# Kernel tuning notes

Hardware: AMD Instinct MI355X
Metric: run time of the kernel (lower is better)

Reference implementation:

```python
import jax, jax.numpy as jnp
import numpy as np


def setup_inputs() -> dict:
    key = jax.random.key(0)
    k1, k2, k3, k4 = jax.random.split(key, 4)
    N, C, H, W = 4, 256, 64, 64
    Co, kh, kw, dg = 256, 3, 3, 1
    x = jax.random.normal(k1, (N, C, H, W), dtype=jnp.float32)
    offset = jax.random.normal(k2, (N, 2 * dg * kh * kw, H, W), dtype=jnp.float32)
    mask = jax.random.uniform(k3, (N, dg * kh * kw, H, W), dtype=jnp.float32)
    weight = jax.random.normal(k4, (Co, C, kh, kw), dtype=jnp.float32) * 0.02
    bias = jnp.zeros((Co,), dtype=jnp.float32)
    return {"x": x, "offset": offset, "mask": mask, "weight": weight, "bias": bias,
            "stride": 1, "padding": 1, "dilation": 1, "deformable_groups": 1}


def _dcn_v2(x, offset, mask, weight, bias, stride, padding, dilation, dg):
    N, C, H, W = x.shape
    Co, Ci, kh, kw = weight.shape
    K = kh * kw
    Ho, Wo = offset.shape[2], offset.shape[3]
    Cg = C // dg

    off = offset.reshape(N, dg, K, 2, Ho, Wo)
    dy, dx = off[:, :, :, 0], off[:, :, :, 1]          # [N,dg,K,Ho,Wo]
    m = mask.reshape(N, dg, K, Ho, Wo)

    ki = (jnp.arange(K) // kw).astype(jnp.float32)      # kernel row index
    kj = (jnp.arange(K) % kw).astype(jnp.float32)       # kernel col index
    base_y = (jnp.arange(Ho, dtype=jnp.float32) * stride - padding)
    base_x = (jnp.arange(Wo, dtype=jnp.float32) * stride - padding)
    # sampling coordinates [N,dg,K,Ho,Wo]
    py = dy + base_y[None, None, None, :, None] + (ki * dilation)[None, None, :, None, None]
    px = dx + base_x[None, None, None, None, :] + (kj * dilation)[None, None, :, None, None]

    y0 = jnp.floor(py)
    x0 = jnp.floor(px)
    wy1 = py - y0
    wx1 = px - x0
    wy0 = 1.0 - wy1
    wx0 = 1.0 - wx1
    y0i = y0.astype(jnp.int32)
    x0i = x0.astype(jnp.int32)

    xr = x.reshape(N, dg, Cg, H * W)

    def gather(yi, xi):
        valid = ((yi >= 0) & (yi < H) & (xi >= 0) & (xi < W)).astype(x.dtype)
        idx = jnp.clip(yi, 0, H - 1) * W + jnp.clip(xi, 0, W - 1)   # [N,dg,K,Ho,Wo]
        flat = idx.reshape(N, dg, 1, K * Ho * Wo)
        g = jnp.take_along_axis(xr, flat, axis=-1).reshape(N, dg, Cg, K, Ho, Wo)
        return g * valid[:, :, None]

    sampled = (gather(y0i, x0i) * (wy0 * wx0)[:, :, None]
               + gather(y0i, x0i + 1) * (wy0 * wx1)[:, :, None]
               + gather(y0i + 1, x0i) * (wy1 * wx0)[:, :, None]
               + gather(y0i + 1, x0i + 1) * (wy1 * wx1)[:, :, None])
    sampled = sampled * m[:, :, None]                     # modulation
    sampled = sampled.reshape(N, C, K, Ho, Wo)

    out = jnp.einsum('nckhw,ock->nohw', sampled, weight.reshape(Co, C, K))
    return out + bias[None, :, None, None]


def reference(x, offset, mask, weight, bias, stride, padding, dilation, deformable_groups):
    return _dcn_v2(x, offset, mask, weight, bias, stride, padding, dilation, deformable_groups)
```

## Files before the change

kernel.cpp:

```cpp
#include <hip/hip_runtime.h>


typedef _Float16 f16x8 __attribute__((ext_vector_type(8)));
typedef _Float16 f16x4 __attribute__((ext_vector_type(4)));
typedef float f32x4 __attribute__((ext_vector_type(4)));

#define C_IN 256
#define CO   256
#define KK   9
#define HWSZ 4096
#define LDB  72
#define BUFB (64 * LDB)

struct __align__(16) SP2 { uint4 off; f16x4 w; };

static __device__ __forceinline__ f16x8 splat8(_Float16 v) {
    f16x8 r = {v, v, v, v, v, v, v, v};
    return r;
}

__global__ void transpose_x_kernel(const float* __restrict__ x,
                                   _Float16* __restrict__ xt) {
    __shared__ float tile[64][65];
    const int n  = blockIdx.z;
    const int p0 = blockIdx.x * 64;
    const int c0 = blockIdx.y * 64;
    const int tx = threadIdx.x & 63;
    const int ty = threadIdx.x >> 6;
    for (int i = 0; i < 16; ++i) {
        int c = ty * 16 + i;
        tile[c][tx] = x[((size_t)(n * C_IN + c0 + c) << 12) + p0 + tx];
    }
    __syncthreads();
    for (int i = 0; i < 16; ++i) {
        int p = ty * 16 + i;
        xt[((size_t)((n << 12) + p0 + p) << 8) + c0 + tx] = (_Float16)tile[tx][p];
    }
}

__global__ void transpose_w_kernel(const float* __restrict__ w,
                                   _Float16* __restrict__ wt2) {
    const int o = blockIdx.x;
    const int c = threadIdx.x;
    const int f = o >> 4, r = o & 15, cc = c >> 5, kq = c & 31;
    for (int kk = 0; kk < KK; ++kk) {
        int q = cc * 9 + kk;
        wt2[((f * 72 + q) * 16 + r) * 32 + kq] =
            (_Float16)w[(o * C_IN + c) * KK + kk];
    }
}

template <int NHALF>
__launch_bounds__(256, 2)
__global__ void dcn_main_kernel(const float* __restrict__ offset,
                                const float* __restrict__ mask,
                                const float* __restrict__ bias,
                                const _Float16* __restrict__ xt,
                                const _Float16* __restrict__ wt2,
                                float* __restrict__ out0,
                                float* __restrict__ out1) {
    constexpr int NS = 36 / NHALF;
    __shared__ SP2 sP[576];
    __shared__ _Float16 sB[2][BUFB];

    const int tid = threadIdx.x;
    const int cpx = (256 * NHALF) >> 3;
    const int lin = blockIdx.x;
    const int id  = (lin & 7) * cpx + (lin >> 3);
    const int half = (NHALF == 2) ? (id >> 8) : 0;
    const int pt   = id & 255;
    const int p0   = pt * 64;
    const int n    = p0 >> 12;
    const int phw0 = p0 & 4095;
    const int cc0  = half * 4;

    for (int t = tid; t < 576; t += 256) {
        int pl = t / 9;
        int k  = t - pl * 9;
        int phw = phw0 + pl;
        int h = phw >> 6, w = phw & 63;
        float dy = offset[(size_t)(n * 18 + 2 * k)     * HWSZ + phw];
        float dx = offset[(size_t)(n * 18 + 2 * k + 1) * HWSZ + phw];
        float mv = mask  [(size_t)(n * 9 + k)          * HWSZ + phw];
        float py = dy + (float)(h - 1 + k / 3);
        float px = dx + (float)(w - 1 + k % 3);
        float y0f = floorf(py), x0f = floorf(px);
        int y0 = (int)y0f, x0 = (int)x0f;
        float wy1 = py - y0f, wx1 = px - x0f;
        float wy0 = 1.f - wy1, wx0 = 1.f - wx1;
        int y1 = y0 + 1, x1 = x0 + 1;
        float vy0 = (y0 >= 0 && y0 < 64) ? 1.f : 0.f;
        float vy1 = (y1 >= 0 && y1 < 64) ? 1.f : 0.f;
        float vx0 = (x0 >= 0 && x0 < 64) ? 1.f : 0.f;
        float vx1 = (x1 >= 0 && x1 < 64) ? 1.f : 0.f;
        int cy0 = min(max(y0, 0), 63), cy1 = min(max(y1, 0), 63);
        int cx0 = min(max(x0, 0), 63), cx1 = min(max(x1, 0), 63);
        SP2 e;
        e.off = make_uint4((unsigned)(cy0 * 64 + cx0) << 9,
                           (unsigned)(cy0 * 64 + cx1) << 9,
                           (unsigned)(cy1 * 64 + cx0) << 9,
                           (unsigned)(cy1 * 64 + cx1) << 9);
        f16x4 wv;
        wv.x = (_Float16)(wy0 * wx0 * mv * vy0 * vx0);
        wv.y = (_Float16)(wy0 * wx1 * mv * vy0 * vx1);
        wv.z = (_Float16)(wy1 * wx0 * mv * vy1 * vx0);
        wv.w = (_Float16)(wy1 * wx1 * mv * vy1 * vx1);
        e.w = wv;
        sP[t] = e;
    }
    __syncthreads();

    const int lane = tid & 63;
    const int wid  = tid >> 6;
    const int l15  = lane & 15;
    const int lhi  = lane >> 4;

    const int pixl  = tid >> 2;
    const int oct   = tid & 3;
    const int pixl9 = pixl * 9;

    const char* xb  = (const char*)(xt + ((size_t)n << 12) * C_IN);
    const char* wtb = (const char*)wt2;

    const int vBe = l15 * LDB + lhi * 8;
    const int vWe = pixl * LDB + oct * 8;
    const unsigned chBase = (unsigned)(cc0 * 64 + oct * 16);

    unsigned voffA[4];
    for (int fm = 0; fm < 4; ++fm) {
        int fglob = wid * 4 + fm;
        voffA[fm] = (unsigned)((fglob * 72 + cc0 * 9) * 1024 + l15 * 64 + lhi * 16);
    }

    f16x8 ga[2][8];
    f16x8 aa[2][8];
    f16x4 gw[2][2];
    f32x4 acc[4][4];
    for (int i = 0; i < 4; ++i)
        for (int j = 0; j < 4; ++j)
            acc[i][j] = (f32x4){0.f, 0.f, 0.f, 0.f};

#define ISSUE_GA(T, SLOT)                                                     \
    {                                                                         \
        const SP2 e0 = sP[pixl9 + (2 * (T)) % 9];                             \
        const SP2 e1 = sP[pixl9 + (2 * (T) + 1) % 9];                         \
        gw[SLOT][0] = e0.w;                                                   \
        gw[SLOT][1] = e1.w;                                                   \
        const unsigned cE = chBase + (unsigned)(((2 * (T)) / 9) * 64);        \
        const unsigned cO = chBase + (unsigned)(((2 * (T) + 1) / 9) * 64);    \
        ga[SLOT][0] = *(const f16x8*)(xb + (e0.off.x + cE));                  \
        ga[SLOT][1] = *(const f16x8*)(xb + (e0.off.y + cE));                  \
        ga[SLOT][2] = *(const f16x8*)(xb + (e0.off.z + cE));                  \
        ga[SLOT][3] = *(const f16x8*)(xb + (e0.off.w + cE));                  \
        ga[SLOT][4] = *(const f16x8*)(xb + (e1.off.x + cO));                  \
        ga[SLOT][5] = *(const f16x8*)(xb + (e1.off.y + cO));                  \
        ga[SLOT][6] = *(const f16x8*)(xb + (e1.off.z + cO));                  \
        ga[SLOT][7] = *(const f16x8*)(xb + (e1.off.w + cO));                  \
    }

#define ISSUE_A(T, SLOT)                                                      \
    {                                                                         \
        for (int fm_ = 0; fm_ < 4; ++fm_) {                                   \
            unsigned vo_ = voffA[fm_] + (unsigned)((T) * 2048);               \
            aa[SLOT][fm_ * 2 + 0] = *(const f16x8*)(wtb + vo_);               \
            aa[SLOT][fm_ * 2 + 1] = *(const f16x8*)(wtb + vo_ + 1024);        \
        }                                                                     \
    }

#define COMBINE(SLOT, BUF)                                                    \
    {                                                                         \
        _Float16* bw_ = &sB[0][0] + (BUF) * BUFB + vWe;                       \
        f16x8 r0_ = ga[SLOT][0] * splat8(gw[SLOT][0].x)                       \
                  + ga[SLOT][1] * splat8(gw[SLOT][0].y)                       \
                  + ga[SLOT][2] * splat8(gw[SLOT][0].z)                       \
                  + ga[SLOT][3] * splat8(gw[SLOT][0].w);                      \
        f16x8 r1_ = ga[SLOT][4] * splat8(gw[SLOT][1].x)                       \
                  + ga[SLOT][5] * splat8(gw[SLOT][1].y)                       \
                  + ga[SLOT][6] * splat8(gw[SLOT][1].z)                       \
                  + ga[SLOT][7] * splat8(gw[SLOT][1].w);                      \
        *(f16x8*)(bw_)      = r0_;                                            \
        *(f16x8*)(bw_ + 32) = r1_;                                            \
    }

#define MFMA_STEP(SLOT, BUF)                                                  \
    {                                                                         \
        const _Float16* br_ = &sB[0][0] + (BUF) * BUFB + vBe;                 \
        for (int fn_ = 0; fn_ < 4; ++fn_) {                                   \
            f16x8 bE_ = *(const f16x8*)(br_ + fn_ * 16 * LDB);                \
            f16x8 bO_ = *(const f16x8*)(br_ + fn_ * 16 * LDB + 32);           \
            for (int fm_ = 0; fm_ < 4; ++fm_) {                               \
                acc[fm_][fn_] = __builtin_amdgcn_mfma_f32_16x16x32_f16(       \
                    aa[SLOT][fm_ * 2 + 0], bE_, acc[fm_][fn_], 0, 0, 0);      \
                acc[fm_][fn_] = __builtin_amdgcn_mfma_f32_16x16x32_f16(       \
                    aa[SLOT][fm_ * 2 + 1], bO_, acc[fm_][fn_], 0, 0, 0);      \
            }                                                                 \
        }                                                                     \
    }

#define BAR()                                                                 \
    {                                                                         \
        asm volatile("s_waitcnt lgkmcnt(0)" ::: "memory");                    \
        __builtin_amdgcn_s_barrier();                                         \
        asm volatile("" ::: "memory");                                        \
    }

    ISSUE_GA(0, 0)
    ISSUE_GA(1, 1)
    ISSUE_A(0, 0)
    COMBINE(0, 0)
    BAR()

#pragma unroll
    for (int s = 0; s < NS; ++s) {
        if (s + 1 < NS) ISSUE_A(s + 1, (s + 1) & 1)
        if (s + 2 < NS) ISSUE_GA(s + 2, s & 1)
        __builtin_amdgcn_sched_barrier(0);
        MFMA_STEP(s & 1, s & 1)
        if (s + 1 < NS) {
            COMBINE((s + 1) & 1, (s + 1) & 1)
            BAR()
        }
    }

    float* po = (NHALF == 2 && half == 1) ? out1 : out0;
    for (int fm = 0; fm < 4; ++fm) {
        for (int fn = 0; fn < 4; ++fn) {
            int pix = phw0 + fn * 16 + l15;
            for (int r = 0; r < 4; ++r) {
                int o = wid * 64 + fm * 16 + lhi * 4 + r;
                float v = acc[fm][fn][r];
                if constexpr (NHALF == 1) v += bias[o];
                po[((size_t)(n * CO + o) << 12) + pix] = v;
            }
        }
    }
#undef ISSUE_GA
#undef ISSUE_A
#undef COMBINE
#undef MFMA_STEP
#undef BAR
}

__global__ void reduce_kernel(float* __restrict__ out,
                              const float* __restrict__ part,
                              const float* __restrict__ bias, int n4) {
    int i = blockIdx.x * blockDim.x + threadIdx.x;
    const int stride = gridDim.x * blockDim.x;
    for (; i < n4; i += stride) {
        f32x4 a = ((const f32x4*)out)[i];
        f32x4 b = ((const f32x4*)part)[i];
        float bv = bias[(i >> 10) & 255];
        a.x += b.x + bv; a.y += b.y + bv; a.z += b.z + bv; a.w += b.w + bv;
        ((f32x4*)out)[i] = a;
    }
}

extern "C" void kernel_launch(void* const* d_in, const int* in_sizes, int n_in,
                              void* d_out, int out_size, void* d_ws, size_t ws_size,
                              hipStream_t stream) {
    const float* x      = (const float*)d_in[0];
    const float* offset = (const float*)d_in[1];
    const float* mask   = (const float*)d_in[2];
    const float* weight = (const float*)d_in[3];
    const float* bias   = (const float*)d_in[4];
    float* out = (float*)d_out;

    _Float16* xt  = (_Float16*)d_ws;
    _Float16* wt2 = (_Float16*)((char*)d_ws + 8388608);
    float*  part1 = (float*)((char*)d_ws + 9568256);
    const bool split = ws_size >= (size_t)9568256 + (size_t)4 * CO * HWSZ * 4;

    transpose_x_kernel<<<dim3(64, 4, 4), 256, 0, stream>>>(x, xt);
    transpose_w_kernel<<<CO, C_IN, 0, stream>>>(weight, wt2);
    if (split) {
        dcn_main_kernel<2><<<dim3(512), 256, 0, stream>>>(offset, mask, bias,
                                                          xt, wt2, out, part1);
        reduce_kernel<<<dim3(2048), 256, 0, stream>>>(out, part1, bias,
                                                      (4 * CO * HWSZ) / 4);
    } else {
        dcn_main_kernel<1><<<dim3(256), 256, 0, stream>>>(offset, mask, bias,
                                                          xt, wt2, out, out);
    }
}
```

Before: 55.34 us.

## Split channel reduction four ways with fp16 partials and higher occupancy

Raises the split-K factor of the deformable conv GEMM from two to four, launching 1024 blocks so more CUs are busy, and raises launch bounds to target four blocks per SM. All four quarters write fp16 partial sums to workspace, and a one-pass reduce kernel sums them with the bias in fp32. Weight fragments are no longer double-buffered in registers, and MFMA sections get raised wave priority. Storing partials in fp16 adds rounding error and extra reduce traffic, and the lower register budget may cause spills or stalls on the weight loads.

```diff
diff --git a/kernel.cpp b/kernel.cpp
--- a/kernel.cpp
+++ b/kernel.cpp
@@ -11,6 +11,7 @@
 #define HWSZ 4096
 #define LDB  72
 #define BUFB (64 * LDB)
+#define PSTR (4 * CO * HWSZ)
 
 struct __align__(16) SP2 { uint4 off; f16x4 w; };
 
@@ -50,29 +51,29 @@
     }
 }
 
-template <int NHALF>
-__launch_bounds__(256, 2)
+template <int NQ>
+__launch_bounds__(256, 4)
 __global__ void dcn_main_kernel(const float* __restrict__ offset,
                                 const float* __restrict__ mask,
                                 const float* __restrict__ bias,
                                 const _Float16* __restrict__ xt,
                                 const _Float16* __restrict__ wt2,
-                                float* __restrict__ out0,
-                                float* __restrict__ out1) {
-    constexpr int NS = 36 / NHALF;
+                                float* __restrict__ out,
+                                _Float16* __restrict__ parts) {
+    constexpr int NS = 36 / NQ;
     __shared__ SP2 sP[576];
     __shared__ _Float16 sB[2][BUFB];
 
     const int tid = threadIdx.x;
-    const int cpx = (256 * NHALF) >> 3;
+    const int cpx = (256 * NQ) >> 3;
     const int lin = blockIdx.x;
     const int id  = (lin & 7) * cpx + (lin >> 3);
-    const int half = (NHALF == 2) ? (id >> 8) : 0;
+    const int quarter = (NQ > 1) ? (id >> 8) : 0;
     const int pt   = id & 255;
     const int p0   = pt * 64;
     const int n    = p0 >> 12;
     const int phw0 = p0 & 4095;
-    const int cc0  = half * 4;
+    const int cc0  = quarter * (8 / NQ);
 
     for (int t = tid; t < 576; t += 256) {
         int pl = t / 9;
@@ -133,7 +134,7 @@
     }
 
     f16x8 ga[2][8];
-    f16x8 aa[2][8];
+    f16x8 aa[8];
     f16x4 gw[2][2];
     f32x4 acc[4][4];
     for (int i = 0; i < 4; ++i)
@@ -158,12 +159,12 @@
         ga[SLOT][7] = *(const f16x8*)(xb + (e1.off.w + cO));                  \
     }
 
-#define ISSUE_A(T, SLOT)                                                      \
+#define ISSUE_A(T)                                                            \
     {                                                                         \
         for (int fm_ = 0; fm_ < 4; ++fm_) {                                   \
             unsigned vo_ = voffA[fm_] + (unsigned)((T) * 2048);               \
-            aa[SLOT][fm_ * 2 + 0] = *(const f16x8*)(wtb + vo_);               \
-            aa[SLOT][fm_ * 2 + 1] = *(const f16x8*)(wtb + vo_ + 1024);        \
+            aa[fm_ * 2 + 0] = *(const f16x8*)(wtb + vo_);                     \
+            aa[fm_ * 2 + 1] = *(const f16x8*)(wtb + vo_ + 1024);              \
         }                                                                     \
     }
 
@@ -182,19 +183,21 @@
         *(f16x8*)(bw_ + 32) = r1_;                                            \
     }
 
-#define MFMA_STEP(SLOT, BUF)                                                  \
+#define MFMA_STEP(BUF)                                                        \
     {                                                                         \
         const _Float16* br_ = &sB[0][0] + (BUF) * BUFB + vBe;                 \
+        __builtin_amdgcn_s_setprio(1);                                        \
         for (int fn_ = 0; fn_ < 4; ++fn_) {                                   \
             f16x8 bE_ = *(const f16x8*)(br_ + fn_ * 16 * LDB);                \
             f16x8 bO_ = *(const f16x8*)(br_ + fn_ * 16 * LDB + 32);           \
             for (int fm_ = 0; fm_ < 4; ++fm_) {                               \
                 acc[fm_][fn_] = __builtin_amdgcn_mfma_f32_16x16x32_f16(       \
-                    aa[SLOT][fm_ * 2 + 0], bE_, acc[fm_][fn_], 0, 0, 0);      \
+                    aa[fm_ * 2 + 0], bE_, acc[fm_][fn_], 0, 0, 0);            \
                 acc[fm_][fn_] = __builtin_amdgcn_mfma_f32_16x16x32_f16(       \
-                    aa[SLOT][fm_ * 2 + 1], bO_, acc[fm_][fn_], 0, 0, 0);      \
+                    aa[fm_ * 2 + 1], bO_, acc[fm_][fn_], 0, 0, 0);            \
             }                                                                 \
         }                                                                     \
+        __builtin_amdgcn_s_setprio(0);                                        \
     }
 
 #define BAR()                                                                 \
@@ -206,31 +209,42 @@
 
     ISSUE_GA(0, 0)
     ISSUE_GA(1, 1)
-    ISSUE_A(0, 0)
     COMBINE(0, 0)
     BAR()
 
 #pragma unroll
     for (int s = 0; s < NS; ++s) {
-        if (s + 1 < NS) ISSUE_A(s + 1, (s + 1) & 1)
+        ISSUE_A(s)
         if (s + 2 < NS) ISSUE_GA(s + 2, s & 1)
         __builtin_amdgcn_sched_barrier(0);
-        MFMA_STEP(s & 1, s & 1)
+        MFMA_STEP(s & 1)
         if (s + 1 < NS) {
             COMBINE((s + 1) & 1, (s + 1) & 1)
             BAR()
         }
     }
 
-    float* po = (NHALF == 2 && half == 1) ? out1 : out0;
-    for (int fm = 0; fm < 4; ++fm) {
-        for (int fn = 0; fn < 4; ++fn) {
-            int pix = phw0 + fn * 16 + l15;
-            for (int r = 0; r < 4; ++r) {
-                int o = wid * 64 + fm * 16 + lhi * 4 + r;
-                float v = acc[fm][fn][r];
-                if constexpr (NHALF == 1) v += bias[o];
-                po[((size_t)(n * CO + o) << 12) + pix] = v;
+    if constexpr (NQ > 1) {
+        _Float16* pp = parts + (size_t)quarter * PSTR;
+        for (int fm = 0; fm < 4; ++fm) {
+            for (int fn = 0; fn < 4; ++fn) {
+                int pix = phw0 + fn * 16 + l15;
+                for (int r = 0; r < 4; ++r) {
+                    int o = wid * 64 + fm * 16 + lhi * 4 + r;
+                    pp[((size_t)(n * CO + o) << 12) + pix] =
+                        (_Float16)acc[fm][fn][r];
+                }
+            }
+        }
+    } else {
+        for (int fm = 0; fm < 4; ++fm) {
+            for (int fn = 0; fn < 4; ++fn) {
+                int pix = phw0 + fn * 16 + l15;
+                for (int r = 0; r < 4; ++r) {
+                    int o = wid * 64 + fm * 16 + lhi * 4 + r;
+                    out[((size_t)(n * CO + o) << 12) + pix] =
+                        acc[fm][fn][r] + bias[o];
+                }
             }
         }
     }
@@ -242,17 +256,22 @@
 }
 
 __global__ void reduce_kernel(float* __restrict__ out,
-                              const float* __restrict__ part,
-                              const float* __restrict__ bias, int n4) {
+                              const _Float16* __restrict__ parts,
+                              const float* __restrict__ bias, int n8) {
     int i = blockIdx.x * blockDim.x + threadIdx.x;
-    const int stride = gridDim.x * blockDim.x;
-    for (; i < n4; i += stride) {
-        f32x4 a = ((const f32x4*)out)[i];
-        f32x4 b = ((const f32x4*)part)[i];
-        float bv = bias[(i >> 10) & 255];
-        a.x += b.x + bv; a.y += b.y + bv; a.z += b.z + bv; a.w += b.w + bv;
-        ((f32x4*)out)[i] = a;
-    }
+    if (i >= n8) return;
+    f16x8 a = ((const f16x8*)parts)[i];
+    f16x8 b = ((const f16x8*)(parts + PSTR))[i];
+    f16x8 c = ((const f16x8*)(parts + 2 * (size_t)PSTR))[i];
+    f16x8 d = ((const f16x8*)(parts + 3 * (size_t)PSTR))[i];
+    float bv = bias[((i * 8) >> 12) & 255];
+    f32x4 r0, r1;
+    for (int e = 0; e < 4; ++e)
+        r0[e] = (float)a[e] + (float)b[e] + (float)c[e] + (float)d[e] + bv;
+    for (int e = 0; e < 4; ++e)
+        r1[e] = (float)a[e+4] + (float)b[e+4] + (float)c[e+4] + (float)d[e+4] + bv;
+    ((f32x4*)out)[2 * i]     = r0;
+    ((f32x4*)out)[2 * i + 1] = r1;
 }
 
 extern "C" void kernel_launch(void* const* d_in, const int* in_sizes, int n_in,
@@ -267,18 +286,18 @@
 
     _Float16* xt  = (_Float16*)d_ws;
     _Float16* wt2 = (_Float16*)((char*)d_ws + 8388608);
-    float*  part1 = (float*)((char*)d_ws + 9568256);
-    const bool split = ws_size >= (size_t)9568256 + (size_t)4 * CO * HWSZ * 4;
+    _Float16* parts = (_Float16*)((char*)d_ws + 9568256);
+    const bool split = ws_size >= (size_t)9568256 + (size_t)4 * PSTR * 2;
 
     transpose_x_kernel<<<dim3(64, 4, 4), 256, 0, stream>>>(x, xt);
     transpose_w_kernel<<<CO, C_IN, 0, stream>>>(weight, wt2);
     if (split) {
-        dcn_main_kernel<2><<<dim3(512), 256, 0, stream>>>(offset, mask, bias,
-                                                          xt, wt2, out, part1);
-        reduce_kernel<<<dim3(2048), 256, 0, stream>>>(out, part1, bias,
-                                                      (4 * CO * HWSZ) / 4);
+        dcn_main_kernel<4><<<dim3(1024), 256, 0, stream>>>(offset, mask, bias,
+                                                           xt, wt2, out, parts);
+        reduce_kernel<<<dim3(PSTR / 8 / 256), 256, 0, stream>>>(out, parts, bias,
+                                                                PSTR / 8);
     } else {
         dcn_main_kernel<1><<<dim3(256), 256, 0, stream>>>(offset, mask, bias,
-                                                          xt, wt2, out, out);
-    }
-}
+                                                          xt, wt2, out, parts);
+    }
+}
```

Measured after the change: 185.9 us. 236% more time.

## Fuse prep kernels with bias init and replace split-K reduce with atomics

Applied to the files above, without the earlier changes.

Merges the x transpose, weight transpose and a new bias-initialisation of the output into one prep kernel launch. The main kernel always splits the channel reduction into two halves and accumulates directly into the output with float atomicAdd. This drops the partial-sum workspace and the separate reduce kernel. The cost is atomic traffic on every output element plus a full output write during prep, and the summation order becomes nondeterministic.

```diff
diff --git a/kernel.cpp b/kernel.cpp
--- a/kernel.cpp
+++ b/kernel.cpp
@@ -19,55 +19,60 @@
     return r;
 }
 
-__global__ void transpose_x_kernel(const float* __restrict__ x,
-                                   _Float16* __restrict__ xt) {
+__global__ void prep_kernel(const float* __restrict__ x,
+                            const float* __restrict__ w,
+                            const float* __restrict__ bias,
+                            _Float16* __restrict__ xt,
+                            _Float16* __restrict__ wt2,
+                            float* __restrict__ out) {
     __shared__ float tile[64][65];
-    const int n  = blockIdx.z;
-    const int p0 = blockIdx.x * 64;
-    const int c0 = blockIdx.y * 64;
-    const int tx = threadIdx.x & 63;
-    const int ty = threadIdx.x >> 6;
-    for (int i = 0; i < 16; ++i) {
-        int c = ty * 16 + i;
-        tile[c][tx] = x[((size_t)(n * C_IN + c0 + c) << 12) + p0 + tx];
-    }
-    __syncthreads();
-    for (int i = 0; i < 16; ++i) {
-        int p = ty * 16 + i;
-        xt[((size_t)((n << 12) + p0 + p) << 8) + c0 + tx] = (_Float16)tile[tx][p];
-    }
-}
-
-__global__ void transpose_w_kernel(const float* __restrict__ w,
-                                   _Float16* __restrict__ wt2) {
-    const int o = blockIdx.x;
-    const int c = threadIdx.x;
-    const int f = o >> 4, r = o & 15, cc = c >> 5, kq = c & 31;
-    for (int kk = 0; kk < KK; ++kk) {
-        int q = cc * 9 + kk;
-        wt2[((f * 72 + q) * 16 + r) * 32 + kq] =
-            (_Float16)w[(o * C_IN + c) * KK + kk];
-    }
-}
-
-template <int NHALF>
+    const int b = blockIdx.x;
+    if (b < 1024) {
+        const int bx = b & 63, by = (b >> 6) & 3, n = b >> 8;
+        const int p0 = bx * 64;
+        const int c0 = by * 64;
+        const int tx = threadIdx.x & 63;
+        const int ty = threadIdx.x >> 6;
+        for (int i = 0; i < 16; ++i) {
+            int c = ty * 16 + i;
+            tile[c][tx] = x[((size_t)(n * C_IN + c0 + c) << 12) + p0 + tx];
+        }
+        __syncthreads();
+        for (int i = 0; i < 16; ++i) {
+            int p = ty * 16 + i;
+            xt[((size_t)((n << 12) + p0 + p) << 8) + c0 + tx] =
+                (_Float16)tile[tx][p];
+        }
+    } else if (b < 1280) {
+        const int o = b - 1024;
+        const int c = threadIdx.x;
+        const int f = o >> 4, r = o & 15, cc = c >> 5, kq = c & 31;
+        for (int kk = 0; kk < KK; ++kk) {
+            int q = cc * 9 + kk;
+            wt2[((f * 72 + q) * 16 + r) * 32 + kq] =
+                (_Float16)w[(o * C_IN + c) * KK + kk];
+        }
+    } else {
+        const int i = (b - 1280) * 256 + threadIdx.x;
+        const float bv = bias[(i >> 10) & 255];
+        ((f32x4*)out)[i] = (f32x4){bv, bv, bv, bv};
+    }
+}
+
 __launch_bounds__(256, 2)
 __global__ void dcn_main_kernel(const float* __restrict__ offset,
                                 const float* __restrict__ mask,
-                                const float* __restrict__ bias,
                                 const _Float16* __restrict__ xt,
                                 const _Float16* __restrict__ wt2,
-                                float* __restrict__ out0,
-                                float* __restrict__ out1) {
-    constexpr int NS = 36 / NHALF;
+                                float* __restrict__ out) {
+    constexpr int NS = 18;
     __shared__ SP2 sP[576];
     __shared__ _Float16 sB[2][BUFB];
 
     const int tid = threadIdx.x;
-    const int cpx = (256 * NHALF) >> 3;
     const int lin = blockIdx.x;
-    const int id  = (lin & 7) * cpx + (lin >> 3);
-    const int half = (NHALF == 2) ? (id >> 8) : 0;
+    const int id  = (lin & 7) * 64 + (lin >> 3);
+    const int half = id >> 8;
     const int pt   = id & 255;
     const int p0   = pt * 64;
     const int n    = p0 >> 12;
@@ -222,37 +227,20 @@
         }
     }
 
-    float* po = (NHALF == 2 && half == 1) ? out1 : out0;
-    for (int fm = 0; fm < 4; ++fm) {
+    for (int fm = 0; fm < 4; ++fm)
         for (int fn = 0; fn < 4; ++fn) {
             int pix = phw0 + fn * 16 + l15;
             for (int r = 0; r < 4; ++r) {
                 int o = wid * 64 + fm * 16 + lhi * 4 + r;
-                float v = acc[fm][fn][r];
-                if constexpr (NHALF == 1) v += bias[o];
-                po[((size_t)(n * CO + o) << 12) + pix] = v;
+                atomicAdd(&out[((size_t)(n * CO + o) << 12) + pix],
+                          acc[fm][fn][r]);
             }
         }
-    }
 #undef ISSUE_GA
 #undef ISSUE_A
 #undef COMBINE
 #undef MFMA_STEP
 #undef BAR
-}
-
-__global__ void reduce_kernel(float* __restrict__ out,
-                              const float* __restrict__ part,
-                              const float* __restrict__ bias, int n4) {
-    int i = blockIdx.x * blockDim.x + threadIdx.x;
-    const int stride = gridDim.x * blockDim.x;
-    for (; i < n4; i += stride) {
-        f32x4 a = ((const f32x4*)out)[i];
-        f32x4 b = ((const f32x4*)part)[i];
-        float bv = bias[(i >> 10) & 255];
-        a.x += b.x + bv; a.y += b.y + bv; a.z += b.z + bv; a.w += b.w + bv;
-        ((f32x4*)out)[i] = a;
-    }
 }
 
 extern "C" void kernel_launch(void* const* d_in, const int* in_sizes, int n_in,
@@ -267,18 +255,8 @@
 
     _Float16* xt  = (_Float16*)d_ws;
     _Float16* wt2 = (_Float16*)((char*)d_ws + 8388608);
-    float*  part1 = (float*)((char*)d_ws + 9568256);
-    const bool split = ws_size >= (size_t)9568256 + (size_t)4 * CO * HWSZ * 4;
-
-    transpose_x_kernel<<<dim3(64, 4, 4), 256, 0, stream>>>(x, xt);
-    transpose_w_kernel<<<CO, C_IN, 0, stream>>>(weight, wt2);
-    if (split) {
-        dcn_main_kernel<2><<<dim3(512), 256, 0, stream>>>(offset, mask, bias,
-                                                          xt, wt2, out, part1);
-        reduce_kernel<<<dim3(2048), 256, 0, stream>>>(out, part1, bias,
-                                                      (4 * CO * HWSZ) / 4);
-    } else {
-        dcn_main_kernel<1><<<dim3(256), 256, 0, stream>>>(offset, mask, bias,
-                                                          xt, wt2, out, out);
-    }
-}
+
+    prep_kernel<<<dim3(1024 + 256 + 4096), 256, 0, stream>>>(x, weight, bias,
+                                                             xt, wt2, out);
+    dcn_main_kernel<<<dim3(512), 256, 0, stream>>>(offset, mask, xt, wt2, out);
+}
```

After: 64.23 us. 1.16x slower.
